# Performance work log

Measured on AMD Instinct MI355X. Metric: run time of the kernel, lower is better.

## Reference

```python
import math
import jax, jax.numpy as jnp
import numpy as np

D = 512; H = 8; N = 6; DFF = 2048; VS = 32000; VT = 32000
B = 4; S = 1024; T = 1024
EPS = 1e-5


def _pe(length, d):
    pos = jnp.arange(length, dtype=jnp.float32)[:, None]
    div = jnp.exp(jnp.arange(0, d, 2, dtype=jnp.float32) * (-math.log(10000.0) / d))
    pe = jnp.zeros((length, d), jnp.float32)
    pe = pe.at[:, 0::2].set(jnp.sin(pos * div)).at[:, 1::2].set(jnp.cos(pos * div))
    return pe  # [L, D]


def _ln(x, g, b):
    m = x.mean(-1, keepdims=True)
    v = ((x - m) ** 2).mean(-1, keepdims=True)
    return (x - m) / jnp.sqrt(v + EPS) * g + b


def _mha(xq, xkv, w, b, mask):
    # w: [4, D, D], b: [4, D]; mask broadcastable to [B, H, Sq, Sk]
    nb, sq, d = xq.shape
    dk = d // H
    def proj(x, i):
        return (x @ w[i] + b[i]).reshape(x.shape[0], x.shape[1], H, dk).transpose(0, 2, 1, 3)
    q, k, v = proj(xq, 0), proj(xkv, 1), proj(xkv, 2)
    scores = jnp.einsum('bhqd,bhkd->bhqk', q, k) / math.sqrt(dk)
    scores = jnp.where(mask == 0, -1e9, scores)
    p = jax.nn.softmax(scores, axis=-1)
    o = jnp.einsum('bhqk,bhkd->bhqd', p, v).transpose(0, 2, 1, 3).reshape(nb, sq, d)
    return o @ w[3] + b[3]


def _ffn(x, w1, b1, w2, b2):
    return jax.nn.relu(x @ w1 + b1) @ w2 + b2


def _forward(src_emb, tgt_emb,
             enc_attn_w, enc_attn_b, enc_ffn_w1, enc_ffn_b1, enc_ffn_w2, enc_ffn_b2,
             enc_ln_g, enc_ln_b, enc_fg, enc_fb,
             dec_self_w, dec_self_b, dec_src_w, dec_src_b,
             dec_ffn_w1, dec_ffn_b1, dec_ffn_w2, dec_ffn_b2,
             dec_ln_g, dec_ln_b, dec_fg, dec_fb,
             gen_w, gen_b,
             src, tgt, src_mask, tgt_mask):
    # embed + positional encoding (dropout off: eval mode)
    x = src_emb[src] + _pe(src.shape[1], D)[None]
    for i in range(N):
        a = _mha(x, x, enc_attn_w[i], enc_attn_b[i], src_mask)
        x = _ln(x + a, enc_ln_g[i, 0], enc_ln_b[i, 0])
        f = _ffn(x, enc_ffn_w1[i], enc_ffn_b1[i], enc_ffn_w2[i], enc_ffn_b2[i])
        x = _ln(x + f, enc_ln_g[i, 1], enc_ln_b[i, 1])
    memory = _ln(x, enc_fg, enc_fb)

    y = tgt_emb[tgt] + _pe(tgt.shape[1], D)[None]
    for i in range(N):
        a = _mha(y, y, dec_self_w[i], dec_self_b[i], tgt_mask)
        y = _ln(y + a, dec_ln_g[i, 0], dec_ln_b[i, 0])
        a = _mha(y, memory, dec_src_w[i], dec_src_b[i], src_mask)
        y = _ln(y + a, dec_ln_g[i, 1], dec_ln_b[i, 1])
        f = _ffn(y, dec_ffn_w1[i], dec_ffn_b1[i], dec_ffn_w2[i], dec_ffn_b2[i])
        y = _ln(y + f, dec_ln_g[i, 2], dec_ln_b[i, 2])
    y = _ln(y, dec_fg, dec_fb)
    return y @ gen_w + gen_b  # [B, T, VT]


def setup_inputs():
    key = jax.random.key(0)
    ks = iter(jax.random.split(key, 48))
    def w(*shape):
        return jax.random.normal(next(ks), shape, dtype=jnp.float32) * 0.02
    inp = {}
    inp['src_emb'] = w(VS, D)
    inp['tgt_emb'] = w(VT, D)
    inp['enc_attn_w'] = w(N, 4, D, D)
    inp['enc_attn_b'] = jnp.zeros((N, 4, D), jnp.float32)
    inp['enc_ffn_w1'] = w(N, D, DFF)
    inp['enc_ffn_b1'] = jnp.zeros((N, DFF), jnp.float32)
    inp['enc_ffn_w2'] = w(N, DFF, D)
    inp['enc_ffn_b2'] = jnp.zeros((N, D), jnp.float32)
    inp['enc_ln_g'] = jnp.ones((N, 2, D), jnp.float32)
    inp['enc_ln_b'] = jnp.zeros((N, 2, D), jnp.float32)
    inp['enc_fg'] = jnp.ones((D,), jnp.float32)
    inp['enc_fb'] = jnp.zeros((D,), jnp.float32)
    inp['dec_self_w'] = w(N, 4, D, D)
    inp['dec_self_b'] = jnp.zeros((N, 4, D), jnp.float32)
    inp['dec_src_w'] = w(N, 4, D, D)
    inp['dec_src_b'] = jnp.zeros((N, 4, D), jnp.float32)
    inp['dec_ffn_w1'] = w(N, D, DFF)
    inp['dec_ffn_b1'] = jnp.zeros((N, DFF), jnp.float32)
    inp['dec_ffn_w2'] = w(N, DFF, D)
    inp['dec_ffn_b2'] = jnp.zeros((N, D), jnp.float32)
    inp['dec_ln_g'] = jnp.ones((N, 3, D), jnp.float32)
    inp['dec_ln_b'] = jnp.zeros((N, 3, D), jnp.float32)
    inp['dec_fg'] = jnp.ones((D,), jnp.float32)
    inp['dec_fb'] = jnp.zeros((D,), jnp.float32)
    inp['gen_w'] = w(D, VT)
    inp['gen_b'] = jnp.zeros((VT,), jnp.float32)
    inp['src'] = jax.random.randint(next(ks), (B, S), 0, VS)
    inp['tgt'] = jax.random.randint(next(ks), (B, T), 0, VT)
    inp['src_mask'] = jnp.ones((B, 1, 1, S), jnp.int32)
    inp['tgt_mask'] = jnp.tril(jnp.ones((T, T), jnp.int32))[None, None]  # causal [1,1,T,T]
    return inp


def reference(src_emb, tgt_emb, enc_attn_w, enc_attn_b, enc_ffn_w1, enc_ffn_b1,
              enc_ffn_w2, enc_ffn_b2, enc_ln_g, enc_ln_b, enc_fg, enc_fb,
              dec_self_w, dec_self_b, dec_src_w, dec_src_b,
              dec_ffn_w1, dec_ffn_b1, dec_ffn_w2, dec_ffn_b2,
              dec_ln_g, dec_ln_b, dec_fg, dec_fb, gen_w, gen_b,
              src, tgt, src_mask, tgt_mask):
    return _forward(src_emb, tgt_emb, enc_attn_w, enc_attn_b, enc_ffn_w1, enc_ffn_b1,
                    enc_ffn_w2, enc_ffn_b2, enc_ln_g, enc_ln_b, enc_fg, enc_fb,
                    dec_self_w, dec_self_b, dec_src_w, dec_src_b,
                    dec_ffn_w1, dec_ffn_b1, dec_ffn_w2, dec_ffn_b2,
                    dec_ln_g, dec_ln_b, dec_fg, dec_fb, gen_w, gen_b,
                    src, tgt, src_mask, tgt_mask)
```

## Files before the change

### kernel.cpp

```cpp
#include <hip/hip_runtime.h>


typedef __bf16 bf16x8 __attribute__((ext_vector_type(8)));
typedef __bf16 bf16x4 __attribute__((ext_vector_type(4)));
typedef float  f32x4  __attribute__((ext_vector_type(4)));

__device__ __forceinline__ void gload_lds16(const void* g, void* l) {
  __builtin_amdgcn_global_load_lds((__attribute__((address_space(1))) void*)g,
                                   (__attribute__((address_space(3))) void*)l,
                                   16, 0, 0);
}

__device__ __forceinline__ void hard_barrier() {
  asm volatile("" ::: "memory");
  __builtin_amdgcn_sched_barrier(0);
  __builtin_amdgcn_s_barrier();
  __builtin_amdgcn_sched_barrier(0);
  asm volatile("" ::: "memory");
}

template<int EPI>
__global__ __launch_bounds__(256)
void gemm_kernel(const __bf16* __restrict__ A, int lda,
                 const __bf16* __restrict__ BT, int ldb,
                 void* __restrict__ Cv, int ldc,
                 const float* __restrict__ bias, int K,
                 __bf16* __restrict__ qb, __bf16* __restrict__ kb,
                 __bf16* __restrict__ vt, int zoff)
{
  constexpr int BM = 128, BN = 64, BK = 64;
  constexpr int WM = 64, WN = 32, FM = 4, FN = 2;
  constexpr int LA = (BM * BK) / 2048;
  constexpr int LB = (BN * BK) / 2048;
  constexpr int SLOT = (BM + BN) * BK;
  __shared__ __bf16 lds[3 * SLOT];
  const int tid  = threadIdx.x;
  const int lane = tid & 63, wave = tid >> 6;
  const int wr = wave >> 1, wc = wave & 1;
  const int bm = blockIdx.x * BM, bn = blockIdx.y * BN;

  auto stage = [&](int slot, int kt) {
    const char* Ag = (const char*)A;
    const char* Bg = (const char*)BT;
    char* base = (char*)(lds + slot * SLOT);
    const long long k0b = (long long)kt * (BK * 2);
#pragma unroll
    for (int i = 0; i < LA; i++) {
      int t = tid + i * 256;
      int row = t >> 3, cb = (t & 7) << 4;
      int src = cb ^ ((row & 7) << 4);
      gload_lds16(Ag + ((long long)(bm + row) * lda) * 2 + k0b + src, base + t * 16);
    }
#pragma unroll
    for (int i = 0; i < LB; i++) {
      int t = tid + i * 256;
      int row = t >> 3, cb = (t & 7) << 4;
      int src = cb ^ ((row & 7) << 4);
      gload_lds16(Bg + ((long long)(bn + row) * ldb) * 2 + k0b + src,
                  base + BM * BK * 2 + t * 16);
    }
  };

  f32x4 acc[FM][FN] = {};
  const int NT = K / BK;

  stage(0, 0);
  stage(1, 1);

  for (int t = 0; t < NT; t++) {
    if (t < NT - 1) {
      asm volatile("s_waitcnt vmcnt(6)" ::: "memory");
    } else {
      asm volatile("s_waitcnt vmcnt(0)" ::: "memory");
    }
    hard_barrier();
    if (t + 2 < NT) stage((t + 2) % 3, t + 2);
    const char* sA = (const char*)(lds + (t % 3) * SLOT);
    const char* sB = sA + BM * BK * 2;
#pragma unroll
    for (int kk = 0; kk < 2; kk++) {
      const int g = kk * 64 + (lane >> 4) * 16;
      bf16x8 af[FM], bfr[FN];
#pragma unroll
      for (int i = 0; i < FM; i++) {
        int row = wr * WM + i * 16 + (lane & 15);
        af[i] = *(const bf16x8*)(sA + row * 128 + (g ^ ((row & 7) << 4)));
      }
#pragma unroll
      for (int j = 0; j < FN; j++) {
        int row = wc * WN + j * 16 + (lane & 15);
        bfr[j] = *(const bf16x8*)(sB + row * 128 + (g ^ ((row & 7) << 4)));
      }
      __builtin_amdgcn_s_setprio(1);
#pragma unroll
      for (int i = 0; i < FM; i++)
#pragma unroll
        for (int j = 0; j < FN; j++)
          acc[i][j] = __builtin_amdgcn_mfma_f32_16x16x32_bf16(af[i], bfr[j], acc[i][j], 0, 0, 0);
      __builtin_amdgcn_s_setprio(0);
    }
  }

#pragma unroll
  for (int i = 0; i < FM; i++) {
#pragma unroll
    for (int j = 0; j < FN; j++) {
      int row0 = bm + wr * WM + i * 16 + (lane >> 4) * 4;
      int col  = bn + wc * WN + j * 16 + (lane & 15);
      float bv = bias ? bias[col] : 0.f;
      if constexpr (EPI == 2) {
        int z = zoff + (col >> 9);
        int cw = col & 511;
        int b = row0 >> 10, s = row0 & 1023;
        int h = cw >> 6, dk = cw & 63;
        long long bh = b * 8 + h;
        if (z == 2) {
          bf16x4 vv;
#pragma unroll
          for (int r = 0; r < 4; r++) vv[r] = (__bf16)(acc[i][j][r] + bv);
          *(bf16x4*)(vt + (bh << 16) + (dk << 10) + s) = vv;
        } else {
          __bf16* dst = (z == 0) ? qb : kb;
          float sc = (z == 0) ? 0.125f : 1.0f;
#pragma unroll
          for (int r = 0; r < 4; r++)
            dst[(bh << 16) + ((long long)(s + r) << 6) + dk] = (__bf16)((acc[i][j][r] + bv) * sc);
        }
      } else if constexpr (EPI == 1) {
        __bf16* C = (__bf16*)Cv;
#pragma unroll
        for (int r = 0; r < 4; r++)
          C[(long long)(row0 + r) * ldc + col] = (__bf16)fmaxf(acc[i][j][r] + bv, 0.f);
      } else {
        float* C = (float*)Cv;
#pragma unroll
        for (int r = 0; r < 4; r++)
          C[(long long)(row0 + r) * ldc + col] = acc[i][j][r] + bv;
      }
    }
  }
}

__global__ __launch_bounds__(256)
void gemm_gen_kernel(const __bf16* __restrict__ A, int lda,
                     const __bf16* __restrict__ BT, int ldb,
                     float* __restrict__ C, int ldc,
                     const float* __restrict__ bias, int K, int nbx)
{
  constexpr int BM = 128, BN = 64, BK = 64;
  constexpr int WM = 64, WN = 32, FM = 4, FN = 2;
  constexpr int LA = (BM * BK) / 2048;
  constexpr int LB = (BN * BK) / 2048;
  constexpr int SLOT = (BM + BN) * BK;
  __shared__ __bf16 lds[3 * SLOT];
  const int tid  = threadIdx.x;
  const int lane = tid & 63, wave = tid >> 6;
  const int wr = wave >> 1, wc = wave & 1;
  const int cpx = gridDim.x >> 3;
  const int wg  = (blockIdx.x & 7) * cpx + (blockIdx.x >> 3);
  const int bm  = (wg % nbx) * BM;
  const int bn  = (wg / nbx) * BN;

  auto stage = [&](int slot, int kt) {
    const char* Ag = (const char*)A;
    const char* Bg = (const char*)BT;
    char* base = (char*)(lds + slot * SLOT);
    const long long k0b = (long long)kt * (BK * 2);
#pragma unroll
    for (int i = 0; i < LA; i++) {
      int t = tid + i * 256;
      int row = t >> 3, cb = (t & 7) << 4;
      int src = cb ^ ((row & 7) << 4);
      gload_lds16(Ag + ((long long)(bm + row) * lda) * 2 + k0b + src, base + t * 16);
    }
#pragma unroll
    for (int i = 0; i < LB; i++) {
      int t = tid + i * 256;
      int row = t >> 3, cb = (t & 7) << 4;
      int src = cb ^ ((row & 7) << 4);
      gload_lds16(Bg + ((long long)(bn + row) * ldb) * 2 + k0b + src,
                  base + BM * BK * 2 + t * 16);
    }
  };

  f32x4 acc[FM][FN] = {};
  const int NT = K / BK;

  stage(0, 0);
  stage(1, 1);

  for (int t = 0; t < NT; t++) {
    if (t < NT - 1) {
      asm volatile("s_waitcnt vmcnt(6)" ::: "memory");
    } else {
      asm volatile("s_waitcnt vmcnt(0)" ::: "memory");
    }
    hard_barrier();
    if (t + 2 < NT) stage((t + 2) % 3, t + 2);
    const char* sA = (const char*)(lds + (t % 3) * SLOT);
    const char* sB = sA + BM * BK * 2;
#pragma unroll
    for (int kk = 0; kk < 2; kk++) {
      const int g = kk * 64 + (lane >> 4) * 16;
      bf16x8 af[FM], bfr[FN];
#pragma unroll
      for (int i = 0; i < FM; i++) {
        int row = wr * WM + i * 16 + (lane & 15);
        af[i] = *(const bf16x8*)(sA + row * 128 + (g ^ ((row & 7) << 4)));
      }
#pragma unroll
      for (int j = 0; j < FN; j++) {
        int row = wc * WN + j * 16 + (lane & 15);
        bfr[j] = *(const bf16x8*)(sB + row * 128 + (g ^ ((row & 7) << 4)));
      }
      __builtin_amdgcn_s_setprio(1);
#pragma unroll
      for (int i = 0; i < FM; i++)
#pragma unroll
        for (int j = 0; j < FN; j++)
          acc[i][j] = __builtin_amdgcn_mfma_f32_16x16x32_bf16(af[i], bfr[j], acc[i][j], 0, 0, 0);
      __builtin_amdgcn_s_setprio(0);
    }
  }

  __syncthreads();
  float* ct = (float*)lds;
#pragma unroll
  for (int i = 0; i < FM; i++) {
#pragma unroll
    for (int j = 0; j < FN; j++) {
      int lrow = wr * WM + i * 16 + (lane >> 4) * 4;
      int lcol = wc * WN + j * 16 + (lane & 15);
      float bv = bias[bn + lcol];
#pragma unroll
      for (int r = 0; r < 4; r++)
        ct[(lrow + r) * 68 + lcol] = acc[i][j][r] + bv;
    }
  }
  __syncthreads();
#pragma unroll
  for (int it = 0; it < 8; it++) {
    int idx = tid + it * 256;
    int row = idx >> 4, c4 = (idx & 15) * 4;
    f32x4 v = *(const f32x4*)(ct + row * 68 + c4);
    *(f32x4*)(C + (long long)(bm + row) * ldc + bn + c4) = v;
  }
}

template<int CAUSAL>
__global__ __launch_bounds__(256)
void flash_kernel(const __bf16* __restrict__ qb, const __bf16* __restrict__ kb,
                  const __bf16* __restrict__ vt, const int* __restrict__ smask,
                  __bf16* __restrict__ Ob)
{
  __shared__ __bf16 lK[2 * 128 * 64];
  __shared__ __bf16 lV[2 * 64 * 128];
  __shared__ __bf16 lP[4][16 * 128];
  const int bh = blockIdx.y;
  const int b = bh >> 3, h = bh & 7;
  const int q0 = blockIdx.x * 64;
  const int tid = threadIdx.x, lane = tid & 63, w = tid >> 6;
  const char* kh = (const char*)(kb + ((long long)bh << 16));
  const char* vh = (const char*)(vt + ((long long)bh << 16));

  auto stageKV = [&](int buf, int t) {
    int k0 = t * 128;
#pragma unroll
    for (int i = 0; i < 4; i++) {
      int c = tid + i * 256;
      int row = c >> 3, cb = (c & 7) << 4;
      int cl = cb ^ ((row & 7) << 4);
      gload_lds16(kh + (long long)(k0 + row) * 128 + cl, (char*)lK + buf * 16384 + c * 16);
    }
#pragma unroll
    for (int i = 0; i < 4; i++) {
      int c = tid + i * 256;
      int row = c >> 4, cb = (c & 15) << 4;
      int cl = cb ^ ((row & 7) << 4);
      gload_lds16(vh + (long long)row * 2048 + (long long)k0 * 2 + cl, (char*)lV + buf * 16384 + c * 16);
    }
  };

  bf16x8 qa[2];
  {
    const __bf16* qrow = qb + ((long long)bh << 16)
                       + (long long)(q0 + w * 16 + (lane & 15)) * 64 + (lane >> 4) * 8;
    qa[0] = *(const bf16x8*)(qrow);
    qa[1] = *(const bf16x8*)(qrow + 32);
  }
  f32x4 oacc[4] = {};
  float m[4], l[4];
#pragma unroll
  for (int r = 0; r < 4; r++) { m[r] = -3e38f; l[r] = 0.f; }

  const int nt = CAUSAL ? (blockIdx.x / 2 + 1) : 8;
  char* lPw = (char*)lP + w * 4096;
  stageKV(0, 0);

  for (int t = 0; t < nt; t++) {
    const int k0 = t * 128;
    __syncthreads();
    if (t + 1 < nt) stageKV((t + 1) & 1, t + 1);
    char* cK = (char*)lK + (t & 1) * 16384;
    char* cV = (char*)lV + (t & 1) * 16384;

    f32x4 sf[8];
#pragma unroll
    for (int f = 0; f < 8; f++) {
      int row = f * 16 + (lane & 15);
      f32x4 s = {};
#pragma unroll
      for (int ks = 0; ks < 2; ks++) {
        int cb = ks * 64 + (lane >> 4) * 16;
        bf16x8 kf = *(const bf16x8*)(cK + row * 128 + (cb ^ ((row & 7) << 4)));
        s = __builtin_amdgcn_mfma_f32_16x16x32_bf16(qa[ks], kf, s, 0, 0, 0);
      }
      sf[f] = s;
    }

    if (!CAUSAL) {
#pragma unroll
      for (int f = 0; f < 8; f++) {
        if (smask[b * 1024 + k0 + f * 16 + (lane & 15)] == 0) {
#pragma unroll
          for (int r = 0; r < 4; r++) sf[f][r] = -1e30f;
        }
      }
    } else if (t == nt - 1) {
#pragma unroll
      for (int f = 0; f < 8; f++) {
        int kc = k0 + f * 16 + (lane & 15);
#pragma unroll
        for (int r = 0; r < 4; r++) {
          int qr = q0 + w * 16 + (lane >> 4) * 4 + r;
          if (kc > qr) sf[f][r] = -1e30f;
        }
      }
    }

    float mt[4], mn[4], cr[4], rs[4];
#pragma unroll
    for (int r = 0; r < 4; r++) {
      float v = sf[0][r];
#pragma unroll
      for (int f = 1; f < 8; f++) v = fmaxf(v, sf[f][r]);
      mt[r] = v;
    }
#pragma unroll
    for (int o = 1; o < 16; o <<= 1)
#pragma unroll
      for (int r = 0; r < 4; r++) mt[r] = fmaxf(mt[r], __shfl_xor(mt[r], o));
#pragma unroll
    for (int r = 0; r < 4; r++) {
      mn[r] = fmaxf(m[r], mt[r]);
      cr[r] = __expf(m[r] - mn[r]);
      m[r]  = mn[r];
      rs[r] = 0.f;
    }
#pragma unroll
    for (int f = 0; f < 8; f++)
#pragma unroll
      for (int r = 0; r < 4; r++) {
        float p = __expf(sf[f][r] - mn[r]);
        sf[f][r] = p;
        rs[r] += p;
      }
#pragma unroll
    for (int o = 1; o < 16; o <<= 1)
#pragma unroll
      for (int r = 0; r < 4; r++) rs[r] += __shfl_xor(rs[r], o);
#pragma unroll
    for (int r = 0; r < 4; r++) l[r] = l[r] * cr[r] + rs[r];
#pragma unroll
    for (int d = 0; d < 4; d++)
#pragma unroll
      for (int r = 0; r < 4; r++) oacc[d][r] *= cr[r];

#pragma unroll
    for (int f = 0; f < 8; f++) {
      int colB = f * 32 + (lane & 15) * 2;
#pragma unroll
      for (int r = 0; r < 4; r++) {
        int row = (lane >> 4) * 4 + r;
        *(__bf16*)(lPw + row * 256 + (colB ^ ((row & 7) << 4))) = (__bf16)sf[f][r];
      }
    }
    asm volatile("s_waitcnt lgkmcnt(0)" ::: "memory");

#pragma unroll
    for (int ks = 0; ks < 4; ks++) {
      int prow = lane & 15;
      int cb = ks * 64 + (lane >> 4) * 16;
      bf16x8 pa = *(const bf16x8*)(lPw + prow * 256 + (cb ^ ((prow & 7) << 4)));
#pragma unroll
      for (int d = 0; d < 4; d++) {
        int vrow = d * 16 + (lane & 15);
        bf16x8 vf = *(const bf16x8*)(cV + vrow * 256 + (cb ^ ((vrow & 7) << 4)));
        oacc[d] = __builtin_amdgcn_mfma_f32_16x16x32_bf16(pa, vf, oacc[d], 0, 0, 0);
      }
    }
  }

  float inv[4];
#pragma unroll
  for (int r = 0; r < 4; r++) inv[r] = 1.f / l[r];
#pragma unroll
  for (int d = 0; d < 4; d++)
#pragma unroll
    for (int r = 0; r < 4; r++) {
      long long row = b * 1024 + q0 + w * 16 + (lane >> 4) * 4 + r;
      Ob[row * 512 + h * 64 + d * 16 + (lane & 15)] = (__bf16)(oacc[d][r] * inv[r]);
    }
}

__global__ void transpose_w_kernel(const float* __restrict__ W, __bf16* __restrict__ WT,
                                   int K, int N)
{
  __shared__ float t[32][33];
  long long mz = (long long)blockIdx.z * K * N;
  W += mz; WT += mz;
  int n0 = blockIdx.x * 32, k0 = blockIdx.y * 32;
  int tx = threadIdx.x, ty = threadIdx.y;
#pragma unroll
  for (int i = 0; i < 32; i += 8)
    t[ty + i][tx] = W[(long long)(k0 + ty + i) * N + (n0 + tx)];
  __syncthreads();
#pragma unroll
  for (int i = 0; i < 32; i += 8)
    WT[(long long)(n0 + ty + i) * K + (k0 + tx)] = (__bf16)t[tx][ty + i];
}

__global__ void embed_kernel(const float* __restrict__ emb, const int* __restrict__ idx,
                             float* __restrict__ X, __bf16* __restrict__ Xb)
{
  int row = blockIdx.x;
  int s   = row & 1023;
  int tok = idx[row];
  int d0  = threadIdx.x * 4;
  float4 e = *(const float4*)(emb + (long long)tok * 512 + d0);
  const float* ep = (const float*)&e;
  float o[4];
#pragma unroll
  for (int j = 0; j < 4; j++) {
    int d = d0 + j;
    float div = expf((float)(d & ~1) * (-9.210340371976184f / 512.f));
    float ang = (float)s * div;
    float pe  = (d & 1) ? cosf(ang) : sinf(ang);
    o[j] = ep[j] + pe;
  }
  *(float4*)(X + (long long)row * 512 + d0) = *(float4*)o;
  bf16x4 ob;
#pragma unroll
  for (int j = 0; j < 4; j++) ob[j] = (__bf16)o[j];
  *(bf16x4*)(Xb + (long long)row * 512 + d0) = ob;
}

__global__ void ln_kernel(const float* __restrict__ Xin, const float* __restrict__ Rin,
                          const float* __restrict__ g, const float* __restrict__ b,
                          float* __restrict__ Xout, __bf16* __restrict__ Xbout)
{
  int row = blockIdx.x, lane = threadIdx.x;
  long long base = (long long)row * 512 + lane * 8;
  float x[8];
  *(float4*)x       = *(const float4*)(Xin + base);
  *(float4*)(x + 4) = *(const float4*)(Xin + base + 4);
  if (Rin) {
    float4 r0 = *(const float4*)(Rin + base);
    float4 r1 = *(const float4*)(Rin + base + 4);
    x[0] += r0.x; x[1] += r0.y; x[2] += r0.z; x[3] += r0.w;
    x[4] += r1.x; x[5] += r1.y; x[6] += r1.z; x[7] += r1.w;
  }
  float s = 0.f;
#pragma unroll
  for (int i = 0; i < 8; i++) s += x[i];
#pragma unroll
  for (int o = 32; o > 0; o >>= 1) s += __shfl_xor(s, o);
  float mean = s * (1.f / 512.f);
  float v = 0.f;
#pragma unroll
  for (int i = 0; i < 8; i++) { x[i] -= mean; v += x[i] * x[i]; }
#pragma unroll
  for (int o = 32; o > 0; o >>= 1) v += __shfl_xor(v, o);
  float inv = rsqrtf(v * (1.f / 512.f) + 1e-5f);
  int d0 = lane * 8;
  float gg[8], bb[8];
  *(float4*)gg       = *(const float4*)(g + d0);
  *(float4*)(gg + 4) = *(const float4*)(g + d0 + 4);
  *(float4*)bb       = *(const float4*)(b + d0);
  *(float4*)(bb + 4) = *(const float4*)(b + d0 + 4);
  float y[8]; bf16x8 yb;
#pragma unroll
  for (int i = 0; i < 8; i++) {
    y[i] = x[i] * inv * gg[i] + bb[i];
    yb[i] = (__bf16)y[i];
  }
  if (Xout) {
    *(float4*)(Xout + base)     = *(float4*)y;
    *(float4*)(Xout + base + 4) = *(float4*)(y + 4);
  }
  *(bf16x8*)(Xbout + base) = yb;
}

extern "C" void kernel_launch(void* const* d_in, const int* in_sizes, int n_in,
                              void* d_out, int out_size, void* d_ws, size_t ws_size,
                              hipStream_t stream)
{
  (void)in_sizes; (void)n_in; (void)out_size; (void)ws_size;
  const float* src_emb    = (const float*)d_in[0];
  const float* tgt_emb    = (const float*)d_in[1];
  const float* enc_attn_w = (const float*)d_in[2];
  const float* enc_attn_b = (const float*)d_in[3];
  const float* enc_ffn_w1 = (const float*)d_in[4];
  const float* enc_ffn_b1 = (const float*)d_in[5];
  const float* enc_ffn_w2 = (const float*)d_in[6];
  const float* enc_ffn_b2 = (const float*)d_in[7];
  const float* enc_ln_g   = (const float*)d_in[8];
  const float* enc_ln_b   = (const float*)d_in[9];
  const float* enc_fg     = (const float*)d_in[10];
  const float* enc_fb     = (const float*)d_in[11];
  const float* dec_self_w = (const float*)d_in[12];
  const float* dec_self_b = (const float*)d_in[13];
  const float* dec_src_w  = (const float*)d_in[14];
  const float* dec_src_b  = (const float*)d_in[15];
  const float* dec_ffn_w1 = (const float*)d_in[16];
  const float* dec_ffn_b1 = (const float*)d_in[17];
  const float* dec_ffn_w2 = (const float*)d_in[18];
  const float* dec_ffn_b2 = (const float*)d_in[19];
  const float* dec_ln_g   = (const float*)d_in[20];
  const float* dec_ln_b   = (const float*)d_in[21];
  const float* dec_fg     = (const float*)d_in[22];
  const float* dec_fb     = (const float*)d_in[23];
  const float* gen_w      = (const float*)d_in[24];
  const float* gen_b      = (const float*)d_in[25];
  const int*   src        = (const int*)d_in[26];
  const int*   tgt        = (const int*)d_in[27];
  const int*   src_mask   = (const int*)d_in[28];

  float* out = (float*)d_out;

  char* wp = (char*)d_ws;
  auto alloc = [&](size_t bytes) { void* p = (void*)wp; wp += (bytes + 255) & ~(size_t)255; return p; };
  __bf16* TWea = (__bf16*)alloc(24ull * 262144 * 2);
  __bf16* TWe1 = (__bf16*)alloc(6ull * 1048576 * 2);
  __bf16* TWe2 = (__bf16*)alloc(6ull * 1048576 * 2);
  __bf16* TWds = (__bf16*)alloc(24ull * 262144 * 2);
  __bf16* TWdx = (__bf16*)alloc(24ull * 262144 * 2);
  __bf16* TWd1 = (__bf16*)alloc(6ull * 1048576 * 2);
  __bf16* TWd2 = (__bf16*)alloc(6ull * 1048576 * 2);
  float*  X    = (float*) alloc(4096ull * 512 * 4);
  __bf16* Xb   = (__bf16*)alloc(4096ull * 512 * 2);
  __bf16* MEMb = (__bf16*)alloc(4096ull * 512 * 2);
  float*  R    = (float*) alloc(4096ull * 512 * 4);
  __bf16* qb   = (__bf16*)alloc(32ull * 1024 * 64 * 2);
  __bf16* kb   = (__bf16*)alloc(32ull * 1024 * 64 * 2);
  __bf16* vt   = (__bf16*)alloc(32ull * 1024 * 64 * 2);
  __bf16* Ob   = (__bf16*)alloc(4096ull * 512 * 2);
  __bf16* Fb   = qb;
  __bf16* GENT = TWea;

  transpose_w_kernel<<<dim3(16, 16, 24), dim3(32, 8), 0, stream>>>(enc_attn_w, TWea, 512, 512);
  transpose_w_kernel<<<dim3(64, 16, 6),  dim3(32, 8), 0, stream>>>(enc_ffn_w1, TWe1, 512, 2048);
  transpose_w_kernel<<<dim3(16, 64, 6),  dim3(32, 8), 0, stream>>>(enc_ffn_w2, TWe2, 2048, 512);
  transpose_w_kernel<<<dim3(16, 16, 24), dim3(32, 8), 0, stream>>>(dec_self_w, TWds, 512, 512);
  transpose_w_kernel<<<dim3(16, 16, 24), dim3(32, 8), 0, stream>>>(dec_src_w,  TWdx, 512, 512);
  transpose_w_kernel<<<dim3(64, 16, 6),  dim3(32, 8), 0, stream>>>(dec_ffn_w1, TWd1, 512, 2048);
  transpose_w_kernel<<<dim3(16, 64, 6),  dim3(32, 8), 0, stream>>>(dec_ffn_w2, TWd2, 2048, 512);

  auto attention = [&](const __bf16* wt, const float* bptr, int causal,
                       const __bf16* Aq, const __bf16* Akv) {
    if (Aq == Akv) {
      gemm_kernel<2><<<dim3(32, 24), 256, 0, stream>>>(
          Aq, 512, wt, 512, nullptr, 0, bptr, 512, qb, kb, vt, 0);
    } else {
      gemm_kernel<2><<<dim3(32, 8), 256, 0, stream>>>(
          Aq, 512, wt, 512, nullptr, 0, bptr, 512, qb, kb, vt, 0);
      gemm_kernel<2><<<dim3(32, 16), 256, 0, stream>>>(
          Akv, 512, wt + 262144, 512, nullptr, 0, bptr + 512, 512, qb, kb, vt, 1);
    }
    if (causal)
      flash_kernel<1><<<dim3(16, 32), 256, 0, stream>>>(qb, kb, vt, nullptr, Ob);
    else
      flash_kernel<0><<<dim3(16, 32), 256, 0, stream>>>(qb, kb, vt, src_mask, Ob);
    gemm_kernel<0><<<dim3(32, 8), 256, 0, stream>>>(
        Ob, 512, wt + 3 * 262144, 512, R, 512, bptr + 3 * 512, 512,
        nullptr, nullptr, nullptr, 0);
  };

  auto ffn = [&](const __bf16* w1t, const float* b1, const __bf16* w2t, const float* b2) {
    gemm_kernel<1><<<dim3(32, 32), 256, 0, stream>>>(
        Xb, 512, w1t, 512, Fb, 2048, b1, 512, nullptr, nullptr, nullptr, 0);
    gemm_kernel<0><<<dim3(32, 8), 256, 0, stream>>>(
        Fb, 2048, w2t, 2048, R, 512, b2, 2048, nullptr, nullptr, nullptr, 0);
  };

  embed_kernel<<<4096, 128, 0, stream>>>(src_emb, src, X, Xb);
  for (int i = 0; i < 6; i++) {
    attention(TWea + (long long)i * 1048576, enc_attn_b + i * 2048, 0, Xb, Xb);
    ln_kernel<<<4096, 64, 0, stream>>>(X, R, enc_ln_g + i * 1024, enc_ln_b + i * 1024, X, Xb);
    ffn(TWe1 + (long long)i * 1048576, enc_ffn_b1 + i * 2048,
        TWe2 + (long long)i * 1048576, enc_ffn_b2 + i * 512);
    ln_kernel<<<4096, 64, 0, stream>>>(X, R, enc_ln_g + i * 1024 + 512, enc_ln_b + i * 1024 + 512, X, Xb);
  }
  ln_kernel<<<4096, 64, 0, stream>>>(X, nullptr, enc_fg, enc_fb, nullptr, MEMb);

  transpose_w_kernel<<<dim3(1000, 16, 1), dim3(32, 8), 0, stream>>>(gen_w, GENT, 512, 32000);

  embed_kernel<<<4096, 128, 0, stream>>>(tgt_emb, tgt, X, Xb);
  for (int i = 0; i < 6; i++) {
    attention(TWds + (long long)i * 1048576, dec_self_b + i * 2048, 1, Xb, Xb);
    ln_kernel<<<4096, 64, 0, stream>>>(X, R, dec_ln_g + i * 1536, dec_ln_b + i * 1536, X, Xb);

    attention(TWdx + (long long)i * 1048576, dec_src_b + i * 2048, 0, Xb, MEMb);
    ln_kernel<<<4096, 64, 0, stream>>>(X, R, dec_ln_g + i * 1536 + 512, dec_ln_b + i * 1536 + 512, X, Xb);

    ffn(TWd1 + (long long)i * 1048576, dec_ffn_b1 + i * 2048,
        TWd2 + (long long)i * 1048576, dec_ffn_b2 + i * 512);
    ln_kernel<<<4096, 64, 0, stream>>>(X, R, dec_ln_g + i * 1536 + 1024, dec_ln_b + i * 1536 + 1024, X, Xb);
  }
  ln_kernel<<<4096, 64, 0, stream>>>(X, nullptr, dec_fg, dec_fb, nullptr, Xb);

  gemm_gen_kernel<<<16000, 256, 0, stream>>>(
      Xb, 512, GENT, 512, out, 32000, gen_b, 512, 32);
}
```

Measured before the change: 2.110 ms.

## Add 128x128-tile double-buffered GEMM for wide-N projections and generator

```diff
diff --git a/kernel.cpp b/kernel.cpp
--- a/kernel.cpp
+++ b/kernel.cpp
@@ -17,6 +17,155 @@
   __builtin_amdgcn_s_barrier();
   __builtin_amdgcn_sched_barrier(0);
   asm volatile("" ::: "memory");
+}
+
+template<int EPI>
+__global__ __launch_bounds__(256)
+void gemm2_kernel(const __bf16* __restrict__ A, int lda,
+                  const __bf16* __restrict__ BT, int ldb,
+                  void* __restrict__ Cv, int ldc,
+                  const float* __restrict__ bias, int K,
+                  __bf16* __restrict__ qb, __bf16* __restrict__ kb,
+                  __bf16* __restrict__ vt, int zoff)
+{
+  constexpr int BM = 128, BN = 128, BK = 64;
+  constexpr int WM = 64, WN = 64, FM = 4, FN = 4;
+  constexpr int SLOT = 2 * BM * BK;
+  __shared__ char ldsraw[69632];
+  __bf16* lds = (__bf16*)ldsraw;
+  const int tid  = threadIdx.x;
+  const int lane = tid & 63, wave = tid >> 6;
+  const int wr = wave >> 1, wc = wave & 1;
+  const int bm = blockIdx.x * BM, bn = blockIdx.y * BN;
+
+  auto stage = [&](int slot, int kt) {
+    const char* Ag = (const char*)A;
+    const char* Bg = (const char*)BT;
+    char* base = (char*)(lds + slot * SLOT);
+    const long long k0b = (long long)kt * (BK * 2);
+#pragma unroll
+    for (int i = 0; i < 4; i++) {
+      int t = tid + i * 256;
+      int row = t >> 3, cb = (t & 7) << 4;
+      int src = cb ^ ((row & 7) << 4);
+      gload_lds16(Ag + ((long long)(bm + row) * lda) * 2 + k0b + src, base + t * 16);
+    }
+#pragma unroll
+    for (int i = 0; i < 4; i++) {
+      int t = tid + i * 256;
+      int row = t >> 3, cb = (t & 7) << 4;
+      int src = cb ^ ((row & 7) << 4);
+      gload_lds16(Bg + ((long long)(bn + row) * ldb) * 2 + k0b + src,
+                  base + BM * BK * 2 + t * 16);
+    }
+  };
+
+  f32x4 acc[FM][FN] = {};
+  const int NT = K / BK;
+
+  stage(0, 0);
+  stage(1, 1);
+
+  for (int t = 0; t < NT; t++) {
+    if (t < NT - 1) {
+      asm volatile("s_waitcnt vmcnt(8)" ::: "memory");
+    } else {
+      asm volatile("s_waitcnt vmcnt(0)" ::: "memory");
+    }
+    hard_barrier();
+    const char* sA = (const char*)(lds + (t & 1) * SLOT);
+    const char* sB = sA + BM * BK * 2;
+#pragma unroll
+    for (int kk = 0; kk < 2; kk++) {
+      const int g = kk * 64 + (lane >> 4) * 16;
+      bf16x8 af[FM], bfr[FN];
+#pragma unroll
+      for (int i = 0; i < FM; i++) {
+        int row = wr * WM + i * 16 + (lane & 15);
+        af[i] = *(const bf16x8*)(sA + row * 128 + (g ^ ((row & 7) << 4)));
+      }
+#pragma unroll
+      for (int j = 0; j < FN; j++) {
+        int row = wc * WN + j * 16 + (lane & 15);
+        bfr[j] = *(const bf16x8*)(sB + row * 128 + (g ^ ((row & 7) << 4)));
+      }
+      __builtin_amdgcn_s_setprio(1);
+#pragma unroll
+      for (int i = 0; i < FM; i++)
+#pragma unroll
+        for (int j = 0; j < FN; j++)
+          acc[i][j] = __builtin_amdgcn_mfma_f32_16x16x32_bf16(af[i], bfr[j], acc[i][j], 0, 0, 0);
+      __builtin_amdgcn_s_setprio(0);
+    }
+    hard_barrier();
+    if (t + 2 < NT) stage(t & 1, t + 2);
+  }
+
+  if constexpr (EPI == 3) {
+    __syncthreads();
+    float* ct = (float*)ldsraw;
+#pragma unroll
+    for (int i = 0; i < FM; i++) {
+#pragma unroll
+      for (int j = 0; j < FN; j++) {
+        int lrow = wr * WM + i * 16 + (lane >> 4) * 4;
+        int lcol = wc * WN + j * 16 + (lane & 15);
+        float bv = bias[bn + lcol];
+#pragma unroll
+        for (int r = 0; r < 4; r++)
+          ct[(lrow + r) * 132 + lcol] = acc[i][j][r] + bv;
+      }
+    }
+    __syncthreads();
+    float* C = (float*)Cv;
+#pragma unroll
+    for (int it = 0; it < 16; it++) {
+      int idx = tid + it * 256;
+      int row = idx >> 5, c4 = (idx & 31) * 4;
+      f32x4 v = *(const f32x4*)(ct + row * 132 + c4);
+      *(f32x4*)(C + (long long)(bm + row) * ldc + bn + c4) = v;
+    }
+    return;
+  }
+
+#pragma unroll
+  for (int i = 0; i < FM; i++) {
+#pragma unroll
+    for (int j = 0; j < FN; j++) {
+      int row0 = bm + wr * WM + i * 16 + (lane >> 4) * 4;
+      int col  = bn + wc * WN + j * 16 + (lane & 15);
+      float bv = bias ? bias[col] : 0.f;
+      if constexpr (EPI == 2) {
+        int z = zoff + (col >> 9);
+        int cw = col & 511;
+        int b = row0 >> 10, s = row0 & 1023;
+        int h = cw >> 6, dk = cw & 63;
+        long long bh = b * 8 + h;
+        if (z == 2) {
+          bf16x4 vv;
+#pragma unroll
+          for (int r = 0; r < 4; r++) vv[r] = (__bf16)(acc[i][j][r] + bv);
+          *(bf16x4*)(vt + (bh << 16) + (dk << 10) + s) = vv;
+        } else {
+          __bf16* dst = (z == 0) ? qb : kb;
+          float sc = (z == 0) ? 0.125f : 1.0f;
+#pragma unroll
+          for (int r = 0; r < 4; r++)
+            dst[(bh << 16) + ((long long)(s + r) << 6) + dk] = (__bf16)((acc[i][j][r] + bv) * sc);
+        }
+      } else if constexpr (EPI == 1) {
+        __bf16* C = (__bf16*)Cv;
+#pragma unroll
+        for (int r = 0; r < 4; r++)
+          C[(long long)(row0 + r) * ldc + col] = (__bf16)fmaxf(acc[i][j][r] + bv, 0.f);
+      } else {
+        float* C = (float*)Cv;
+#pragma unroll
+        for (int r = 0; r < 4; r++)
+          C[(long long)(row0 + r) * ldc + col] = acc[i][j][r] + bv;
+      }
+    }
+  }
 }
 
 template<int EPI>
@@ -126,11 +275,6 @@
           for (int r = 0; r < 4; r++)
             dst[(bh << 16) + ((long long)(s + r) << 6) + dk] = (__bf16)((acc[i][j][r] + bv) * sc);
         }
-      } else if constexpr (EPI == 1) {
-        __bf16* C = (__bf16*)Cv;
-#pragma unroll
-        for (int r = 0; r < 4; r++)
-          C[(long long)(row0 + r) * ldc + col] = (__bf16)fmaxf(acc[i][j][r] + bv, 0.f);
       } else {
         float* C = (float*)Cv;
 #pragma unroll
@@ -138,112 +282,6 @@
           C[(long long)(row0 + r) * ldc + col] = acc[i][j][r] + bv;
       }
     }
-  }
-}
-
-__global__ __launch_bounds__(256)
-void gemm_gen_kernel(const __bf16* __restrict__ A, int lda,
-                     const __bf16* __restrict__ BT, int ldb,
-                     float* __restrict__ C, int ldc,
-                     const float* __restrict__ bias, int K, int nbx)
-{
-  constexpr int BM = 128, BN = 64, BK = 64;
-  constexpr int WM = 64, WN = 32, FM = 4, FN = 2;
-  constexpr int LA = (BM * BK) / 2048;
-  constexpr int LB = (BN * BK) / 2048;
-  constexpr int SLOT = (BM + BN) * BK;
-  __shared__ __bf16 lds[3 * SLOT];
-  const int tid  = threadIdx.x;
-  const int lane = tid & 63, wave = tid >> 6;
-  const int wr = wave >> 1, wc = wave & 1;
-  const int cpx = gridDim.x >> 3;
-  const int wg  = (blockIdx.x & 7) * cpx + (blockIdx.x >> 3);
-  const int bm  = (wg % nbx) * BM;
-  const int bn  = (wg / nbx) * BN;
-
-  auto stage = [&](int slot, int kt) {
-    const char* Ag = (const char*)A;
-    const char* Bg = (const char*)BT;
-    char* base = (char*)(lds + slot * SLOT);
-    const long long k0b = (long long)kt * (BK * 2);
-#pragma unroll
-    for (int i = 0; i < LA; i++) {
-      int t = tid + i * 256;
-      int row = t >> 3, cb = (t & 7) << 4;
-      int src = cb ^ ((row & 7) << 4);
-      gload_lds16(Ag + ((long long)(bm + row) * lda) * 2 + k0b + src, base + t * 16);
-    }
-#pragma unroll
-    for (int i = 0; i < LB; i++) {
-      int t = tid + i * 256;
-      int row = t >> 3, cb = (t & 7) << 4;
-      int src = cb ^ ((row & 7) << 4);
-      gload_lds16(Bg + ((long long)(bn + row) * ldb) * 2 + k0b + src,
-                  base + BM * BK * 2 + t * 16);
-    }
-  };
-
-  f32x4 acc[FM][FN] = {};
-  const int NT = K / BK;
-
-  stage(0, 0);
-  stage(1, 1);
-
-  for (int t = 0; t < NT; t++) {
-    if (t < NT - 1) {
-      asm volatile("s_waitcnt vmcnt(6)" ::: "memory");
-    } else {
-      asm volatile("s_waitcnt vmcnt(0)" ::: "memory");
-    }
-    hard_barrier();
-    if (t + 2 < NT) stage((t + 2) % 3, t + 2);
-    const char* sA = (const char*)(lds + (t % 3) * SLOT);
-    const char* sB = sA + BM * BK * 2;
-#pragma unroll
-    for (int kk = 0; kk < 2; kk++) {
-      const int g = kk * 64 + (lane >> 4) * 16;
-      bf16x8 af[FM], bfr[FN];
-#pragma unroll
-      for (int i = 0; i < FM; i++) {
-        int row = wr * WM + i * 16 + (lane & 15);
-        af[i] = *(const bf16x8*)(sA + row * 128 + (g ^ ((row & 7) << 4)));
-      }
-#pragma unroll
-      for (int j = 0; j < FN; j++) {
-        int row = wc * WN + j * 16 + (lane & 15);
-        bfr[j] = *(const bf16x8*)(sB + row * 128 + (g ^ ((row & 7) << 4)));
-      }
-      __builtin_amdgcn_s_setprio(1);
-#pragma unroll
-      for (int i = 0; i < FM; i++)
-#pragma unroll
-        for (int j = 0; j < FN; j++)
-          acc[i][j] = __builtin_amdgcn_mfma_f32_16x16x32_bf16(af[i], bfr[j], acc[i][j], 0, 0, 0);
-      __builtin_amdgcn_s_setprio(0);
-    }
-  }
-
-  __syncthreads();
-  float* ct = (float*)lds;
-#pragma unroll
-  for (int i = 0; i < FM; i++) {
-#pragma unroll
-    for (int j = 0; j < FN; j++) {
-      int lrow = wr * WM + i * 16 + (lane >> 4) * 4;
-      int lcol = wc * WN + j * 16 + (lane & 15);
-      float bv = bias[bn + lcol];
-#pragma unroll
-      for (int r = 0; r < 4; r++)
-        ct[(lrow + r) * 68 + lcol] = acc[i][j][r] + bv;
-    }
-  }
-  __syncthreads();
-#pragma unroll
-  for (int it = 0; it < 8; it++) {
-    int idx = tid + it * 256;
-    int row = idx >> 4, c4 = (idx & 15) * 4;
-    f32x4 v = *(const f32x4*)(ct + row * 68 + c4);
-    *(f32x4*)(C + (long long)(bm + row) * ldc + bn + c4) = v;
   }
 }
 
@@ -569,12 +607,12 @@
   auto attention = [&](const __bf16* wt, const float* bptr, int causal,
                        const __bf16* Aq, const __bf16* Akv) {
     if (Aq == Akv) {
-      gemm_kernel<2><<<dim3(32, 24), 256, 0, stream>>>(
+      gemm2_kernel<2><<<dim3(32, 12), 256, 0, stream>>>(
           Aq, 512, wt, 512, nullptr, 0, bptr, 512, qb, kb, vt, 0);
     } else {
       gemm_kernel<2><<<dim3(32, 8), 256, 0, stream>>>(
           Aq, 512, wt, 512, nullptr, 0, bptr, 512, qb, kb, vt, 0);
-      gemm_kernel<2><<<dim3(32, 16), 256, 0, stream>>>(
+      gemm2_kernel<2><<<dim3(32, 8), 256, 0, stream>>>(
           Akv, 512, wt + 262144, 512, nullptr, 0, bptr + 512, 512, qb, kb, vt, 1);
     }
     if (causal)
@@ -587,7 +625,7 @@
   };
 
   auto ffn = [&](const __bf16* w1t, const float* b1, const __bf16* w2t, const float* b2) {
-    gemm_kernel<1><<<dim3(32, 32), 256, 0, stream>>>(
+    gemm2_kernel<1><<<dim3(32, 16), 256, 0, stream>>>(
         Xb, 512, w1t, 512, Fb, 2048, b1, 512, nullptr, nullptr, nullptr, 0);
     gemm_kernel<0><<<dim3(32, 8), 256, 0, stream>>>(
         Fb, 2048, w2t, 2048, R, 512, b2, 2048, nullptr, nullptr, nullptr, 0);
@@ -619,6 +657,6 @@
   }
   ln_kernel<<<4096, 64, 0, stream>>>(X, nullptr, dec_fg, dec_fb, nullptr, Xb);
 
-  gemm_gen_kernel<<<16000, 256, 0, stream>>>(
-      Xb, 512, GENT, 512, out, 32000, gen_b, 512, 32);
-}
+  gemm2_kernel<3><<<dim3(32, 250), 256, 0, stream>>>(
+      Xb, 512, GENT, 512, out, 32000, gen_b, 512, nullptr, nullptr, nullptr, 0);
+}
```

Measured after the change: 1.962 ms. -7.0%, faster.
